# Optimization experiments

Hardware: AMD Instinct MI355X
Metric: run time of the kernel (lower is better)

Reference implementation:

```python
import jax, jax.numpy as jnp
import numpy as np

N_TOKENS = 4096
HIDDEN = 1024
FFN = 2048
N_EXPERTS = 8
TOP_K = 2


def setup_inputs() -> dict:
    key = jax.random.key(0)
    k1, k2, k3, k4 = jax.random.split(key, 4)
    x = jax.random.normal(k1, (N_TOKENS, HIDDEN), dtype=jnp.float32)
    router_weight = jax.random.normal(k2, (HIDDEN, N_EXPERTS), dtype=jnp.float32)
    # matches torch.randn(...) * 0.02 init scale
    w1 = jax.random.normal(k3, (HIDDEN, FFN * N_EXPERTS), dtype=jnp.float32) * 0.02
    w2 = jax.random.normal(k4, (FFN * N_EXPERTS, HIDDEN), dtype=jnp.float32) * 0.02
    return {"x": x, "router_weight": router_weight, "w1": w1, "w2": w2, "top_k": TOP_K}


def reference(x, router_weight, w1, w2, top_k):
    # x: [N, H]; router_weight: [H, E]; w1: [H, E*F]; w2: [E*F, H]
    N, H = x.shape
    E = router_weight.shape[1]
    F = w1.shape[1] // E

    # --- routing (router in fp32, softmax over experts, top-k probs) ---
    logits = x.astype(jnp.float32) @ router_weight            # [N, E]
    probs = jax.nn.softmax(logits, axis=-1)                   # [N, E]
    topk_probs, topk_idx = jax.lax.top_k(probs, top_k)        # [N, k]

    # --- expert FFN: per-expert gelu(x @ w1_e) @ w2_e ---
    # Dense formulation: compute every expert for every token, then gather the
    # top-k outputs per token. Same math as grouped-GEMM dispatch/combine.
    h = jax.nn.gelu(x @ w1, approximate=False)                # [N, E*F]
    h = h.reshape(N, E, F)
    w2e = w2.reshape(E, F, H)
    y = jnp.einsum('nef,efh->neh', h, w2e)                    # [N, E, H]

    # --- combine: weight selected expert outputs by router probs, sum top-k ---
    sel = jnp.take_along_axis(y, topk_idx[:, :, None], axis=1)   # [N, k, H]
    out = (sel * topk_probs[:, :, None].astype(sel.dtype)).sum(axis=1)  # [N, H]
    return out
```

## Files before the change

kernel.cpp:

```cpp
#include <hip/hip_runtime.h>
#include <hip/hip_bf16.h>
#include <math.h>

#define N_TOK 4096
#define HID   1024
#define FFN   2048
#define NEXP  8
#define WROW  (NEXP*FFN)
#define NSLOT (N_TOK*2)
#define NCHUNK (NSLOT/64)

typedef __attribute__((ext_vector_type(4))) float f32x4;
typedef __attribute__((ext_vector_type(8))) short short8;

__device__ inline unsigned short f2bf(float f) {
  union { float f; unsigned u; } v; v.f = f;
  unsigned r = v.u + 0x7fffu + ((v.u >> 16) & 1u);
  return (unsigned short)(r >> 16);
}

__device__ __forceinline__ void gload16(const void* g, void* l) {
  __builtin_amdgcn_global_load_lds((const __attribute__((address_space(1))) void*)g,
                                   (__attribute__((address_space(3))) void*)l, 16, 0, 0);
}

__global__ __launch_bounds__(256) void router_kernel(
    const float* __restrict__ x, const float* __restrict__ rw,
    int* __restrict__ eidx, float* __restrict__ probs,
    unsigned short* __restrict__ xb) {
  __shared__ float rwT[NEXP][HID];
  const int t = threadIdx.x;
  #pragma unroll
  for (int it = 0; it < 8; ++it) {
    const int flat = t * 4 + it * 1024;
    const f32x4 v = *(const f32x4*)&rw[flat];
    #pragma unroll
    for (int j = 0; j < 4; ++j) rwT[(flat + j) & 7][(flat + j) >> 3] = v[j];
  }
  __syncthreads();

  const int w = t >> 6, l = t & 63;
  const int n = blockIdx.x * 4 + w;
  const float* xr = x + (size_t)n * HID;
  float acc[NEXP];
  #pragma unroll
  for (int e = 0; e < NEXP; ++e) acc[e] = 0.f;

  #pragma unroll
  for (int j = 0; j < 4; ++j) {
    const int i = l * 4 + j * 256;
    const f32x4 xv = *(const f32x4*)&xr[i];
    if (xb) {
      ushort4 o;
      o.x = f2bf(xv[0]); o.y = f2bf(xv[1]); o.z = f2bf(xv[2]); o.w = f2bf(xv[3]);
      *(ushort4*)&xb[(size_t)n * HID + i] = o;
    }
    #pragma unroll
    for (int e = 0; e < NEXP; ++e) {
      const f32x4 wv = *(const f32x4*)&rwT[e][i];
      acc[e] += xv[0] * wv[0] + xv[1] * wv[1] + xv[2] * wv[2] + xv[3] * wv[3];
    }
  }
  #pragma unroll
  for (int e = 0; e < NEXP; ++e) {
    float s = acc[e];
    #pragma unroll
    for (int off = 32; off; off >>= 1) s += __shfl_xor(s, off);
    acc[e] = s;
  }
  if (l == 0) {
    float m = acc[0];
    #pragma unroll
    for (int e = 1; e < NEXP; ++e) m = fmaxf(m, acc[e]);
    float p[NEXP]; float den = 0.f;
    #pragma unroll
    for (int e = 0; e < NEXP; ++e) { p[e] = expf(acc[e] - m); den += p[e]; }
    const float inv = 1.f / den;
    int e1 = 0; float b1 = -1.f;
    #pragma unroll
    for (int e = 0; e < NEXP; ++e) if (p[e] > b1) { b1 = p[e]; e1 = e; }
    int e2 = 0; float b2 = -1.f;
    #pragma unroll
    for (int e = 0; e < NEXP; ++e) if (e != e1 && p[e] > b2) { b2 = p[e]; e2 = e; }
    eidx[n * 2 + 0] = e1; eidx[n * 2 + 1] = e2;
    probs[n * 2 + 0] = b1 * inv; probs[n * 2 + 1] = b2 * inv;
  }
}

__global__ __launch_bounds__(256) void dispatch_kernel(
    const int* __restrict__ eidx, const float* __restrict__ probs,
    int* __restrict__ counts, int* __restrict__ offs,
    int* __restrict__ rowtok, float* __restrict__ rowprob) {
  __shared__ int chunkbase[NCHUNK][NEXP];
  __shared__ int tot[NEXP], off_s[NEXP];
  const int t = threadIdx.x;
  const int w = t >> 6, l = t & 63;

  for (int c = w; c < NCHUNK; c += 4) {
    const int e = eidx[c * 64 + l];
    #pragma unroll
    for (int xp = 0; xp < NEXP; ++xp) {
      const unsigned long long m = __ballot(e == xp);
      if (l == xp) chunkbase[c][xp] = __popcll(m);
    }
  }
  __syncthreads();

  if (t < NEXP) {
    int a = 0;
    for (int c = 0; c < NCHUNK; ++c) {
      const int v = chunkbase[c][t];
      chunkbase[c][t] = a;
      a += v;
    }
    tot[t] = a;
  }
  __syncthreads();
  if (t == 0) {
    int a = 0;
    for (int e = 0; e < NEXP; ++e) { off_s[e] = a; offs[e] = a; counts[e] = tot[e]; a += tot[e]; }
  }
  __syncthreads();

  for (int c = w; c < NCHUNK; c += 4) {
    const int s = c * 64 + l;
    const int e = eidx[s];
    unsigned long long mask_e = 0;
    #pragma unroll
    for (int xp = 0; xp < NEXP; ++xp) {
      const unsigned long long m = __ballot(e == xp);
      if (e == xp) mask_e = m;
    }
    const unsigned long long below = mask_e & ((1ull << l) - 1ull);
    const int pos = off_s[e] + chunkbase[c][e] + __popcll(below);
    rowtok[pos]  = s >> 1;
    rowprob[pos] = probs[s];
  }
}

__global__ __launch_bounds__(256) void tconv_kernel(
    const float* __restrict__ in, unsigned short* __restrict__ out,
    int R, int C, int RB) {
  __shared__ float tile[64][65];
  const int r0 = blockIdx.y * 64, c0 = blockIdx.x * 64;
  const int t = threadIdx.x;
  const int tr = t >> 4;
  const int tc4 = (t & 15) * 4;
  #pragma unroll
  for (int i = 0; i < 4; ++i) {
    const int r = tr + i * 16;
    const f32x4 v = *(const f32x4*)&in[(size_t)(r0 + r) * C + c0 + tc4];
    tile[r][tc4 + 0] = v[0]; tile[r][tc4 + 1] = v[1];
    tile[r][tc4 + 2] = v[2]; tile[r][tc4 + 3] = v[3];
  }
  __syncthreads();
  const int eb  = r0 / RB;
  const int rm0 = r0 % RB;
  #pragma unroll
  for (int i = 0; i < 4; ++i) {
    const int c = tr + i * 16;
    ushort4 o;
    o.x = f2bf(tile[tc4 + 0][c]); o.y = f2bf(tile[tc4 + 1][c]);
    o.z = f2bf(tile[tc4 + 2][c]); o.w = f2bf(tile[tc4 + 3][c]);
    const size_t oidx = (size_t)eb * C * RB + (size_t)(c0 + c) * RB + rm0 + tc4;
    *(ushort4*)&out[oidx] = o;
  }
}

__global__ __launch_bounds__(256) void gemm1_fast(
    const unsigned short* __restrict__ xb, const unsigned short* __restrict__ w1t,
    const int* __restrict__ rowtok, const int* __restrict__ counts,
    const int* __restrict__ offs, unsigned short* __restrict__ h1) {
  const int e   = blockIdx.z;
  const int cnt = counts[e];
  const int m0  = blockIdx.y * 128;
  if (m0 >= cnt) return;
  const int n0  = blockIdx.x * 128;
  const int seg = offs[e];

  __shared__ alignas(16) unsigned short Al[128 * 32];
  __shared__ alignas(16) unsigned short Bl[128 * 32];

  const int t  = threadIdx.x;
  const int l  = t & 63;
  const int w  = t >> 6;
  const int wr = w >> 1, wc = w & 1;
  const int lr = l & 15, hi = l >> 4;

  const int rowS = t >> 2;
  const int kc   = (t & 3) * 8;
  const int ra0 = m0 + rowS      < cnt ? m0 + rowS      : cnt - 1;
  const int ra1 = m0 + rowS + 64 < cnt ? m0 + rowS + 64 : cnt - 1;
  const unsigned short* aptr0 = xb + (size_t)rowtok[seg + ra0] * HID + kc;
  const unsigned short* aptr1 = xb + (size_t)rowtok[seg + ra1] * HID + kc;
  const unsigned short* bptr0 = w1t + ((size_t)e * FFN + n0 + rowS)      * HID + kc;
  const unsigned short* bptr1 = w1t + ((size_t)e * FFN + n0 + rowS + 64) * HID + kc;
  unsigned short* const ldsA0 = Al + (t & 192) * 8;
  unsigned short* const ldsB0 = Bl + (t & 192) * 8;

  f32x4 acc[4][4];
  #pragma unroll
  for (int i = 0; i < 4; ++i)
    #pragma unroll
    for (int j = 0; j < 4; ++j) acc[i][j] = (f32x4){0.f, 0.f, 0.f, 0.f};

  for (int k0 = 0; k0 < HID; k0 += 32) {
    gload16(aptr0 + k0, ldsA0);
    gload16(aptr1 + k0, ldsA0 + 2048);
    gload16(bptr0 + k0, ldsB0);
    gload16(bptr1 + k0, ldsB0 + 2048);
    __syncthreads();
    short8 af[4], bfr[4];
    #pragma unroll
    for (int mi = 0; mi < 4; ++mi) af[mi]  = *(const short8*)&Al[(wr * 64 + mi * 16 + lr) * 32 + hi * 8];
    #pragma unroll
    for (int ni = 0; ni < 4; ++ni) bfr[ni] = *(const short8*)&Bl[(wc * 64 + ni * 16 + lr) * 32 + hi * 8];
    #pragma unroll
    for (int mi = 0; mi < 4; ++mi)
      #pragma unroll
      for (int ni = 0; ni < 4; ++ni)
        acc[mi][ni] = __builtin_amdgcn_mfma_f32_16x16x32_bf16(af[mi], bfr[ni], acc[mi][ni], 0, 0, 0);
    __syncthreads();
  }

  #pragma unroll
  for (int mi = 0; mi < 4; ++mi) {
    #pragma unroll
    for (int r = 0; r < 4; ++r) {
      const int grow = m0 + wr * 64 + mi * 16 + hi * 4 + r;
      if (grow < cnt) {
        const size_t rowoff = (size_t)(seg + grow) * FFN + n0 + wc * 64 + lr;
        #pragma unroll
        for (int ni = 0; ni < 4; ++ni) {
          const float v = acc[mi][ni][r];
          const float g = 0.5f * v * (1.0f + erff(v * 0.70710678118654752f));
          h1[rowoff + ni * 16] = f2bf(g);
        }
      }
    }
  }
}

__global__ __launch_bounds__(256) void gemm2_fast(
    const unsigned short* __restrict__ h1, const unsigned short* __restrict__ w2t,
    const int* __restrict__ rowtok, const float* __restrict__ rowprob,
    const int* __restrict__ counts, const int* __restrict__ offs,
    float* __restrict__ out) {
  const int e   = blockIdx.z;
  const int cnt = counts[e];
  const int m0  = blockIdx.y * 128;
  if (m0 >= cnt) return;
  const int n0  = blockIdx.x * 128;
  const int seg = offs[e];

  __shared__ alignas(16) unsigned short Al[128 * 32];
  __shared__ alignas(16) unsigned short Bl[128 * 32];

  const int t  = threadIdx.x;
  const int l  = t & 63;
  const int w  = t >> 6;
  const int wr = w >> 1, wc = w & 1;
  const int lr = l & 15, hi = l >> 4;

  const int rowS = t >> 2;
  const int kc   = (t & 3) * 8;
  const int ra0 = m0 + rowS      < cnt ? m0 + rowS      : cnt - 1;
  const int ra1 = m0 + rowS + 64 < cnt ? m0 + rowS + 64 : cnt - 1;
  const unsigned short* aptr0 = h1 + (size_t)(seg + ra0) * FFN + kc;
  const unsigned short* aptr1 = h1 + (size_t)(seg + ra1) * FFN + kc;
  const unsigned short* bptr0 = w2t + ((size_t)e * HID + n0 + rowS)      * FFN + kc;
  const unsigned short* bptr1 = w2t + ((size_t)e * HID + n0 + rowS + 64) * FFN + kc;
  unsigned short* const ldsA0 = Al + (t & 192) * 8;
  unsigned short* const ldsB0 = Bl + (t & 192) * 8;

  f32x4 acc[4][4];
  #pragma unroll
  for (int i = 0; i < 4; ++i)
    #pragma unroll
    for (int j = 0; j < 4; ++j) acc[i][j] = (f32x4){0.f, 0.f, 0.f, 0.f};

  for (int k0 = 0; k0 < FFN; k0 += 32) {
    gload16(aptr0 + k0, ldsA0);
    gload16(aptr1 + k0, ldsA0 + 2048);
    gload16(bptr0 + k0, ldsB0);
    gload16(bptr1 + k0, ldsB0 + 2048);
    __syncthreads();
    short8 af[4], bfr[4];
    #pragma unroll
    for (int mi = 0; mi < 4; ++mi) af[mi]  = *(const short8*)&Al[(wr * 64 + mi * 16 + lr) * 32 + hi * 8];
    #pragma unroll
    for (int ni = 0; ni < 4; ++ni) bfr[ni] = *(const short8*)&Bl[(wc * 64 + ni * 16 + lr) * 32 + hi * 8];
    #pragma unroll
    for (int mi = 0; mi < 4; ++mi)
      #pragma unroll
      for (int ni = 0; ni < 4; ++ni)
        acc[mi][ni] = __builtin_amdgcn_mfma_f32_16x16x32_bf16(af[mi], bfr[ni], acc[mi][ni], 0, 0, 0);
    __syncthreads();
  }

  #pragma unroll
  for (int mi = 0; mi < 4; ++mi) {
    #pragma unroll
    for (int r = 0; r < 4; ++r) {
      const int grow = m0 + wr * 64 + mi * 16 + hi * 4 + r;
      if (grow < cnt) {
        const int slot = seg + grow;
        const int tok  = rowtok[slot];
        const float p  = rowprob[slot];
        #pragma unroll
        for (int ni = 0; ni < 4; ++ni)
          atomicAdd(&out[(size_t)tok * HID + n0 + wc * 64 + ni * 16 + lr], p * acc[mi][ni][r]);
      }
    }
  }
}

__global__ __launch_bounds__(256) void gemm1_old(
    const float* __restrict__ x, const float* __restrict__ w1,
    const int* __restrict__ rowtok, const int* __restrict__ counts,
    const int* __restrict__ offs, unsigned short* __restrict__ h1) {
  const int e   = blockIdx.z;
  const int cnt = counts[e];
  const int m0  = blockIdx.y * 64;
  if (m0 >= cnt) return;
  const int n0  = blockIdx.x * 64;
  const int seg = offs[e];
  __shared__ unsigned short Al[64 * 40];
  __shared__ unsigned short Bl[64 * 40];
  const int t  = threadIdx.x;
  const int l  = t & 63;
  const int wv = t >> 6;
  const int wr = wv >> 1, wc = wv & 1;
  const int am  = t >> 2;
  const int akb = (t & 3) * 8;
  const int amg = m0 + am;
  const bool aval = (amg < cnt);
  const float* aptr = aval ? (x + (size_t)rowtok[seg + amg] * HID + akb) : x;
  const int bn  = t & 63;
  const int bkg = (t >> 6) * 8;
  const float* bptr = w1 + (size_t)e * FFN + n0 + bn;
  f32x4 acc[2][2];
  #pragma unroll
  for (int i = 0; i < 2; ++i)
    #pragma unroll
    for (int j = 0; j < 2; ++j) acc[i][j] = (f32x4){0.f, 0.f, 0.f, 0.f};
  const int kreg = (l >> 4) * 8;
  const int lr   = l & 15;
  for (int k0 = 0; k0 < HID; k0 += 32) {
    short8 av = (short8){0,0,0,0,0,0,0,0};
    if (aval) {
      const f32x4 v0 = *(const f32x4*)(aptr + k0);
      const f32x4 v1 = *(const f32x4*)(aptr + k0 + 4);
      #pragma unroll
      for (int j = 0; j < 4; ++j) { av[j] = (short)f2bf(v0[j]); av[4 + j] = (short)f2bf(v1[j]); }
    }
    *(short8*)&Al[am * 40 + akb] = av;
    short8 bv;
    #pragma unroll
    for (int j = 0; j < 8; ++j) bv[j] = (short)f2bf(bptr[(size_t)(k0 + bkg + j) * WROW]);
    *(short8*)&Bl[bn * 40 + bkg] = bv;
    __syncthreads();
    short8 af[2], bfr[2];
    #pragma unroll
    for (int mi = 0; mi < 2; ++mi) af[mi]  = *(const short8*)&Al[(wr * 32 + mi * 16 + lr) * 40 + kreg];
    #pragma unroll
    for (int ni = 0; ni < 2; ++ni) bfr[ni] = *(const short8*)&Bl[(wc * 32 + ni * 16 + lr) * 40 + kreg];
    #pragma unroll
    for (int mi = 0; mi < 2; ++mi)
      #pragma unroll
      for (int ni = 0; ni < 2; ++ni)
        acc[mi][ni] = __builtin_amdgcn_mfma_f32_16x16x32_bf16(af[mi], bfr[ni], acc[mi][ni], 0, 0, 0);
    __syncthreads();
  }
  const int kq = l >> 4;
  #pragma unroll
  for (int mi = 0; mi < 2; ++mi) {
    #pragma unroll
    for (int r = 0; r < 4; ++r) {
      const int grow = m0 + wr * 32 + mi * 16 + kq * 4 + r;
      if (grow < cnt) {
        #pragma unroll
        for (int ni = 0; ni < 2; ++ni) {
          const float v = acc[mi][ni][r];
          const float g = 0.5f * v * (1.0f + erff(v * 0.70710678118654752f));
          h1[(size_t)(seg + grow) * FFN + n0 + wc * 32 + ni * 16 + lr] = f2bf(g);
        }
      }
    }
  }
}

__global__ __launch_bounds__(256) void gemm2_old(
    const unsigned short* __restrict__ h1, const float* __restrict__ w2,
    const int* __restrict__ rowtok, const float* __restrict__ rowprob,
    const int* __restrict__ counts, const int* __restrict__ offs,
    float* __restrict__ out) {
  const int e   = blockIdx.z;
  const int cnt = counts[e];
  const int m0  = blockIdx.y * 64;
  if (m0 >= cnt) return;
  const int n0  = blockIdx.x * 64;
  const int seg = offs[e];
  __shared__ unsigned short Al[64 * 40];
  __shared__ unsigned short Bl[64 * 40];
  const int t  = threadIdx.x;
  const int l  = t & 63;
  const int wv = t >> 6;
  const int wr = wv >> 1, wc = wv & 1;
  const int am  = t >> 2;
  const int akb = (t & 3) * 8;
  const int amg = m0 + am;
  const bool aval = (amg < cnt);
  const unsigned short* aptr = aval ? (h1 + (size_t)(seg + amg) * FFN + akb) : h1;
  const int bn  = t & 63;
  const int bkg = (t >> 6) * 8;
  const float* bptr = w2 + (size_t)e * FFN * HID + n0 + bn;
  f32x4 acc[2][2];
  #pragma unroll
  for (int i = 0; i < 2; ++i)
    #pragma unroll
    for (int j = 0; j < 2; ++j) acc[i][j] = (f32x4){0.f, 0.f, 0.f, 0.f};
  const int kreg = (l >> 4) * 8;
  const int lr   = l & 15;
  for (int k0 = 0; k0 < FFN; k0 += 32) {
    short8 av = (short8){0,0,0,0,0,0,0,0};
    if (aval) av = *(const short8*)(aptr + k0);
    *(short8*)&Al[am * 40 + akb] = av;
    short8 bv;
    #pragma unroll
    for (int j = 0; j < 8; ++j) bv[j] = (short)f2bf(bptr[(size_t)(k0 + bkg + j) * HID]);
    *(short8*)&Bl[bn * 40 + bkg] = bv;
    __syncthreads();
    short8 af[2], bfr[2];
    #pragma unroll
    for (int mi = 0; mi < 2; ++mi) af[mi]  = *(const short8*)&Al[(wr * 32 + mi * 16 + lr) * 40 + kreg];
    #pragma unroll
    for (int ni = 0; ni < 2; ++ni) bfr[ni] = *(const short8*)&Bl[(wc * 32 + ni * 16 + lr) * 40 + kreg];
    #pragma unroll
    for (int mi = 0; mi < 2; ++mi)
      #pragma unroll
      for (int ni = 0; ni < 2; ++ni)
        acc[mi][ni] = __builtin_amdgcn_mfma_f32_16x16x32_bf16(af[mi], bfr[ni], acc[mi][ni], 0, 0, 0);
    __syncthreads();
  }
  const int kq = l >> 4;
  #pragma unroll
  for (int mi = 0; mi < 2; ++mi) {
    #pragma unroll
    for (int r = 0; r < 4; ++r) {
      const int grow = m0 + wr * 32 + mi * 16 + kq * 4 + r;
      if (grow < cnt) {
        const int slot = seg + grow;
        const int tok  = rowtok[slot];
        const float p  = rowprob[slot];
        #pragma unroll
        for (int ni = 0; ni < 2; ++ni)
          atomicAdd(&out[(size_t)tok * HID + n0 + wc * 32 + ni * 16 + lr], p * acc[mi][ni][r]);
      }
    }
  }
}

extern "C" void kernel_launch(void* const* d_in, const int* in_sizes, int n_in,
                              void* d_out, int out_size, void* d_ws, size_t ws_size,
                              hipStream_t stream) {
  const float* x  = (const float*)d_in[0];
  const float* rw = (const float*)d_in[1];
  const float* w1 = (const float*)d_in[2];
  const float* w2 = (const float*)d_in[3];
  float* out = (float*)d_out;

  int*   counts  = (int*)d_ws;
  int*   cursors = counts + 8;
  int*   offs    = counts + 16;
  int*   eidx    = counts + 32;
  float* probs   = (float*)(eidx + NSLOT);
  int*   rowtok  = (int*)(probs + NSLOT);
  float* rowprob = (float*)(rowtok + NSLOT);
  unsigned short* h1 = (unsigned short*)(rowprob + NSLOT);
  unsigned short* xb = h1 + (size_t)NSLOT * FFN;
  unsigned short* wt = xb + (size_t)N_TOK * HID;
  const size_t need_fast = (size_t)((char*)(wt + (size_t)WROW * HID) - (char*)d_ws);
  const bool fast = (ws_size >= need_fast);
  (void)cursors;

  hipMemsetAsync(d_out, 0, (size_t)out_size * sizeof(float), stream);

  router_kernel<<<N_TOK / 4, 256, 0, stream>>>(x, rw, eidx, probs, fast ? xb : nullptr);
  dispatch_kernel<<<1, 256, 0, stream>>>(eidx, probs, counts, offs, rowtok, rowprob);

  if (fast) {
    tconv_kernel<<<dim3(WROW / 64, HID / 64), 256, 0, stream>>>(w1, wt, HID, WROW, HID);
    gemm1_fast<<<dim3(FFN / 128, NSLOT / 128, NEXP), 256, 0, stream>>>(xb, wt, rowtok, counts, offs, h1);
    tconv_kernel<<<dim3(HID / 64, WROW / 64), 256, 0, stream>>>(w2, wt, WROW, HID, FFN);
    gemm2_fast<<<dim3(HID / 128, NSLOT / 128, NEXP), 256, 0, stream>>>(h1, wt, rowtok, rowprob, counts, offs, out);
  } else {
    gemm1_old<<<dim3(FFN / 64, NSLOT / 64, NEXP), 256, 0, stream>>>(x, w1, rowtok, counts, offs, h1);
    gemm2_old<<<dim3(HID / 64, NSLOT / 64, NEXP), 256, 0, stream>>>(h1, w2, rowtok, rowprob, counts, offs, out);
  }
}
```

Measured before the change: 223.5 us.

## Double-buffer LDS in both expert GEMMs and split-K gemm2 across two halves

Both grouped GEMM kernels now use two LDS buffers, so the global-to-LDS loads for the next K slice are issued while MFMAs run on the current slice. This hides memory latency that the single-buffer loop exposed behind a barrier. gemm2 also splits its K dimension (FFN) into two halves across the grid z dimension, doubling block count to improve occupancy. The existing atomicAdd epilogue combines the partial sums, at the cost of twice the atomic traffic on the output.

```diff
diff --git a/kernel.cpp b/kernel.cpp
--- a/kernel.cpp
+++ b/kernel.cpp
@@ -178,8 +178,8 @@
   const int n0  = blockIdx.x * 128;
   const int seg = offs[e];
 
-  __shared__ alignas(16) unsigned short Al[128 * 32];
-  __shared__ alignas(16) unsigned short Bl[128 * 32];
+  __shared__ alignas(16) unsigned short Al[2][128 * 32];
+  __shared__ alignas(16) unsigned short Bl[2][128 * 32];
 
   const int t  = threadIdx.x;
   const int l  = t & 63;
@@ -195,8 +195,7 @@
   const unsigned short* aptr1 = xb + (size_t)rowtok[seg + ra1] * HID + kc;
   const unsigned short* bptr0 = w1t + ((size_t)e * FFN + n0 + rowS)      * HID + kc;
   const unsigned short* bptr1 = w1t + ((size_t)e * FFN + n0 + rowS + 64) * HID + kc;
-  unsigned short* const ldsA0 = Al + (t & 192) * 8;
-  unsigned short* const ldsB0 = Bl + (t & 192) * 8;
+  const int ldst = (t & 192) * 8;
 
   f32x4 acc[4][4];
   #pragma unroll
@@ -204,22 +203,33 @@
     #pragma unroll
     for (int j = 0; j < 4; ++j) acc[i][j] = (f32x4){0.f, 0.f, 0.f, 0.f};
 
-  for (int k0 = 0; k0 < HID; k0 += 32) {
-    gload16(aptr0 + k0, ldsA0);
-    gload16(aptr1 + k0, ldsA0 + 2048);
-    gload16(bptr0 + k0, ldsB0);
-    gload16(bptr1 + k0, ldsB0 + 2048);
-    __syncthreads();
+  auto STAGE = [&](int b, int k0) {
+    gload16(aptr0 + k0, &Al[b][ldst]);
+    gload16(aptr1 + k0, &Al[b][ldst + 2048]);
+    gload16(bptr0 + k0, &Bl[b][ldst]);
+    gload16(bptr1 + k0, &Bl[b][ldst + 2048]);
+  };
+  auto COMPUTE = [&](int b) {
     short8 af[4], bfr[4];
     #pragma unroll
-    for (int mi = 0; mi < 4; ++mi) af[mi]  = *(const short8*)&Al[(wr * 64 + mi * 16 + lr) * 32 + hi * 8];
-    #pragma unroll
-    for (int ni = 0; ni < 4; ++ni) bfr[ni] = *(const short8*)&Bl[(wc * 64 + ni * 16 + lr) * 32 + hi * 8];
+    for (int mi = 0; mi < 4; ++mi) af[mi]  = *(const short8*)&Al[b][(wr * 64 + mi * 16 + lr) * 32 + hi * 8];
+    #pragma unroll
+    for (int ni = 0; ni < 4; ++ni) bfr[ni] = *(const short8*)&Bl[b][(wc * 64 + ni * 16 + lr) * 32 + hi * 8];
     #pragma unroll
     for (int mi = 0; mi < 4; ++mi)
       #pragma unroll
       for (int ni = 0; ni < 4; ++ni)
         acc[mi][ni] = __builtin_amdgcn_mfma_f32_16x16x32_bf16(af[mi], bfr[ni], acc[mi][ni], 0, 0, 0);
+  };
+
+  STAGE(0, 0);
+  __syncthreads();
+  for (int k0 = 0; k0 < HID; k0 += 64) {
+    STAGE(1, k0 + 32);
+    COMPUTE(0);
+    __syncthreads();
+    if (k0 + 64 < HID) STAGE(0, k0 + 64);
+    COMPUTE(1);
     __syncthreads();
   }
 
@@ -246,15 +256,17 @@
     const int* __restrict__ rowtok, const float* __restrict__ rowprob,
     const int* __restrict__ counts, const int* __restrict__ offs,
     float* __restrict__ out) {
-  const int e   = blockIdx.z;
+  const int e   = blockIdx.z & 7;
+  const int kz  = blockIdx.z >> 3;
   const int cnt = counts[e];
   const int m0  = blockIdx.y * 128;
   if (m0 >= cnt) return;
   const int n0  = blockIdx.x * 128;
   const int seg = offs[e];
-
-  __shared__ alignas(16) unsigned short Al[128 * 32];
-  __shared__ alignas(16) unsigned short Bl[128 * 32];
+  const int kbase = kz * (FFN / 2);
+
+  __shared__ alignas(16) unsigned short Al[2][128 * 32];
+  __shared__ alignas(16) unsigned short Bl[2][128 * 32];
 
   const int t  = threadIdx.x;
   const int l  = t & 63;
@@ -266,12 +278,11 @@
   const int kc   = (t & 3) * 8;
   const int ra0 = m0 + rowS      < cnt ? m0 + rowS      : cnt - 1;
   const int ra1 = m0 + rowS + 64 < cnt ? m0 + rowS + 64 : cnt - 1;
-  const unsigned short* aptr0 = h1 + (size_t)(seg + ra0) * FFN + kc;
-  const unsigned short* aptr1 = h1 + (size_t)(seg + ra1) * FFN + kc;
-  const unsigned short* bptr0 = w2t + ((size_t)e * HID + n0 + rowS)      * FFN + kc;
-  const unsigned short* bptr1 = w2t + ((size_t)e * HID + n0 + rowS + 64) * FFN + kc;
-  unsigned short* const ldsA0 = Al + (t & 192) * 8;
-  unsigned short* const ldsB0 = Bl + (t & 192) * 8;
+  const unsigned short* aptr0 = h1 + (size_t)(seg + ra0) * FFN + kbase + kc;
+  const unsigned short* aptr1 = h1 + (size_t)(seg + ra1) * FFN + kbase + kc;
+  const unsigned short* bptr0 = w2t + ((size_t)e * HID + n0 + rowS)      * FFN + kbase + kc;
+  const unsigned short* bptr1 = w2t + ((size_t)e * HID + n0 + rowS + 64) * FFN + kbase + kc;
+  const int ldst = (t & 192) * 8;
 
   f32x4 acc[4][4];
   #pragma unroll
@@ -279,22 +290,34 @@
     #pragma unroll
     for (int j = 0; j < 4; ++j) acc[i][j] = (f32x4){0.f, 0.f, 0.f, 0.f};
 
-  for (int k0 = 0; k0 < FFN; k0 += 32) {
-    gload16(aptr0 + k0, ldsA0);
-    gload16(aptr1 + k0, ldsA0 + 2048);
-    gload16(bptr0 + k0, ldsB0);
-    gload16(bptr1 + k0, ldsB0 + 2048);
-    __syncthreads();
+  auto STAGE = [&](int b, int k0) {
+    gload16(aptr0 + k0, &Al[b][ldst]);
+    gload16(aptr1 + k0, &Al[b][ldst + 2048]);
+    gload16(bptr0 + k0, &Bl[b][ldst]);
+    gload16(bptr1 + k0, &Bl[b][ldst + 2048]);
+  };
+  auto COMPUTE = [&](int b) {
     short8 af[4], bfr[4];
     #pragma unroll
-    for (int mi = 0; mi < 4; ++mi) af[mi]  = *(const short8*)&Al[(wr * 64 + mi * 16 + lr) * 32 + hi * 8];
-    #pragma unroll
-    for (int ni = 0; ni < 4; ++ni) bfr[ni] = *(const short8*)&Bl[(wc * 64 + ni * 16 + lr) * 32 + hi * 8];
+    for (int mi = 0; mi < 4; ++mi) af[mi]  = *(const short8*)&Al[b][(wr * 64 + mi * 16 + lr) * 32 + hi * 8];
+    #pragma unroll
+    for (int ni = 0; ni < 4; ++ni) bfr[ni] = *(const short8*)&Bl[b][(wc * 64 + ni * 16 + lr) * 32 + hi * 8];
     #pragma unroll
     for (int mi = 0; mi < 4; ++mi)
       #pragma unroll
       for (int ni = 0; ni < 4; ++ni)
         acc[mi][ni] = __builtin_amdgcn_mfma_f32_16x16x32_bf16(af[mi], bfr[ni], acc[mi][ni], 0, 0, 0);
+  };
+
+  STAGE(0, 0);
+  __syncthreads();
+  const int KLEN = FFN / 2;
+  for (int k0 = 0; k0 < KLEN; k0 += 64) {
+    STAGE(1, k0 + 32);
+    COMPUTE(0);
+    __syncthreads();
+    if (k0 + 64 < KLEN) STAGE(0, k0 + 64);
+    COMPUTE(1);
     __syncthreads();
   }
 
@@ -493,7 +516,7 @@
     tconv_kernel<<<dim3(WROW / 64, HID / 64), 256, 0, stream>>>(w1, wt, HID, WROW, HID);
     gemm1_fast<<<dim3(FFN / 128, NSLOT / 128, NEXP), 256, 0, stream>>>(xb, wt, rowtok, counts, offs, h1);
     tconv_kernel<<<dim3(HID / 64, WROW / 64), 256, 0, stream>>>(w2, wt, WROW, HID, FFN);
-    gemm2_fast<<<dim3(HID / 128, NSLOT / 128, NEXP), 256, 0, stream>>>(h1, wt, rowtok, rowprob, counts, offs, out);
+    gemm2_fast<<<dim3(HID / 128, NSLOT / 128, NEXP * 2), 256, 0, stream>>>(h1, wt, rowtok, rowprob, counts, offs, out);
   } else {
     gemm1_old<<<dim3(FFN / 64, NSLOT / 64, NEXP), 256, 0, stream>>>(x, w1, rowtok, counts, offs, h1);
     gemm2_old<<<dim3(HID / 64, NSLOT / 64, NEXP), 256, 0, stream>>>(h1, w2, rowtok, rowprob, counts, offs, out);
```

Measured after the change: 252.9 us. 1.13x slower.

## Replace atomic scatter in expert GEMM2 with split-K bf16 partials and combine kernel

Applied to the files above, without the earlier changes.

The second expert GEMM now writes per-slot bf16 partial outputs, with K split in two for more blocks, instead of atomically adding into the output. A new combine kernel gathers each token's two slots through a token-to-slot map, weights them by the router probabilities and writes the output directly, so the output memset is no longer needed. This removes fp32 atomic contention and raises the block count for the GEMM. It costs an extra launch and extra workspace traffic, and rounding partials to bf16 adds error.

```diff
diff --git a/kernel.cpp b/kernel.cpp
--- a/kernel.cpp
+++ b/kernel.cpp
@@ -18,6 +18,9 @@
   unsigned r = v.u + 0x7fffu + ((v.u >> 16) & 1u);
   return (unsigned short)(r >> 16);
 }
+__device__ __forceinline__ float bf2f(unsigned short u) {
+  union { unsigned u; float f; } v; v.u = ((unsigned)u) << 16; return v.f;
+}
 
 __device__ __forceinline__ void gload16(const void* g, void* l) {
   __builtin_amdgcn_global_load_lds((const __attribute__((address_space(1))) void*)g,
@@ -90,7 +93,8 @@
 __global__ __launch_bounds__(256) void dispatch_kernel(
     const int* __restrict__ eidx, const float* __restrict__ probs,
     int* __restrict__ counts, int* __restrict__ offs,
-    int* __restrict__ rowtok, float* __restrict__ rowprob) {
+    int* __restrict__ rowtok, float* __restrict__ rowprob,
+    int* __restrict__ tokslot) {
   __shared__ int chunkbase[NCHUNK][NEXP];
   __shared__ int tot[NEXP], off_s[NEXP];
   const int t = threadIdx.x;
@@ -135,6 +139,7 @@
     const int pos = off_s[e] + chunkbase[c][e] + __popcll(below);
     rowtok[pos]  = s >> 1;
     rowprob[pos] = probs[s];
+    tokslot[s]   = pos;
   }
 }
 
@@ -241,7 +246,104 @@
   }
 }
 
+template<int KS>
 __global__ __launch_bounds__(256) void gemm2_fast(
+    const unsigned short* __restrict__ h1, const unsigned short* __restrict__ w2t,
+    const int* __restrict__ counts, const int* __restrict__ offs,
+    unsigned short* __restrict__ y) {
+  const int e   = blockIdx.z & 7;
+  const int kz  = blockIdx.z >> 3;
+  const int cnt = counts[e];
+  const int m0  = blockIdx.y * 128;
+  if (m0 >= cnt) return;
+  const int n0  = blockIdx.x * 128;
+  const int seg = offs[e];
+  constexpr int KLEN = FFN / KS;
+  const int kbase = kz * KLEN;
+
+  __shared__ alignas(16) unsigned short Al[128 * 32];
+  __shared__ alignas(16) unsigned short Bl[128 * 32];
+
+  const int t  = threadIdx.x;
+  const int l  = t & 63;
+  const int w  = t >> 6;
+  const int wr = w >> 1, wc = w & 1;
+  const int lr = l & 15, hi = l >> 4;
+
+  const int rowS = t >> 2;
+  const int kc   = (t & 3) * 8;
+  const int ra0 = m0 + rowS      < cnt ? m0 + rowS      : cnt - 1;
+  const int ra1 = m0 + rowS + 64 < cnt ? m0 + rowS + 64 : cnt - 1;
+  const unsigned short* aptr0 = h1 + (size_t)(seg + ra0) * FFN + kbase + kc;
+  const unsigned short* aptr1 = h1 + (size_t)(seg + ra1) * FFN + kbase + kc;
+  const unsigned short* bptr0 = w2t + ((size_t)e * HID + n0 + rowS)      * FFN + kbase + kc;
+  const unsigned short* bptr1 = w2t + ((size_t)e * HID + n0 + rowS + 64) * FFN + kbase + kc;
+  unsigned short* const ldsA0 = Al + (t & 192) * 8;
+  unsigned short* const ldsB0 = Bl + (t & 192) * 8;
+
+  f32x4 acc[4][4];
+  #pragma unroll
+  for (int i = 0; i < 4; ++i)
+    #pragma unroll
+    for (int j = 0; j < 4; ++j) acc[i][j] = (f32x4){0.f, 0.f, 0.f, 0.f};
+
+  for (int k0 = 0; k0 < KLEN; k0 += 32) {
+    gload16(aptr0 + k0, ldsA0);
+    gload16(aptr1 + k0, ldsA0 + 2048);
+    gload16(bptr0 + k0, ldsB0);
+    gload16(bptr1 + k0, ldsB0 + 2048);
+    __syncthreads();
+    short8 af[4], bfr[4];
+    #pragma unroll
+    for (int mi = 0; mi < 4; ++mi) af[mi]  = *(const short8*)&Al[(wr * 64 + mi * 16 + lr) * 32 + hi * 8];
+    #pragma unroll
+    for (int ni = 0; ni < 4; ++ni) bfr[ni] = *(const short8*)&Bl[(wc * 64 + ni * 16 + lr) * 32 + hi * 8];
+    #pragma unroll
+    for (int mi = 0; mi < 4; ++mi)
+      #pragma unroll
+      for (int ni = 0; ni < 4; ++ni)
+        acc[mi][ni] = __builtin_amdgcn_mfma_f32_16x16x32_bf16(af[mi], bfr[ni], acc[mi][ni], 0, 0, 0);
+    __syncthreads();
+  }
+
+  #pragma unroll
+  for (int mi = 0; mi < 4; ++mi) {
+    #pragma unroll
+    for (int r = 0; r < 4; ++r) {
+      const int grow = m0 + wr * 64 + mi * 16 + hi * 4 + r;
+      if (grow < cnt) {
+        const int slot = seg + grow;
+        unsigned short* yrow = y + ((size_t)kz * NSLOT + slot) * HID + n0 + wc * 64 + lr;
+        #pragma unroll
+        for (int ni = 0; ni < 4; ++ni)
+          yrow[ni * 16] = f2bf(acc[mi][ni][r]);
+      }
+    }
+  }
+}
+
+template<int KS>
+__global__ __launch_bounds__(256) void combine_kernel(
+    const unsigned short* __restrict__ y, const int* __restrict__ tokslot,
+    const float* __restrict__ probs, float* __restrict__ out) {
+  const int n = blockIdx.x;
+  const int c = threadIdx.x * 4;
+  const int s1 = tokslot[n * 2 + 0], s2 = tokslot[n * 2 + 1];
+  const float p1 = probs[n * 2 + 0], p2 = probs[n * 2 + 1];
+  float r0 = 0.f, r1 = 0.f, r2 = 0.f, r3 = 0.f;
+  #pragma unroll
+  for (int kz = 0; kz < KS; ++kz) {
+    const ushort4 a = *(const ushort4*)&y[((size_t)kz * NSLOT + s1) * HID + c];
+    const ushort4 b = *(const ushort4*)&y[((size_t)kz * NSLOT + s2) * HID + c];
+    r0 += p1 * bf2f(a.x) + p2 * bf2f(b.x);
+    r1 += p1 * bf2f(a.y) + p2 * bf2f(b.y);
+    r2 += p1 * bf2f(a.z) + p2 * bf2f(b.z);
+    r3 += p1 * bf2f(a.w) + p2 * bf2f(b.w);
+  }
+  *(f32x4*)&out[(size_t)n * HID + c] = (f32x4){r0, r1, r2, r3};
+}
+
+__global__ __launch_bounds__(256) void gemm2_fast_atomic(
     const unsigned short* __restrict__ h1, const unsigned short* __restrict__ w2t,
     const int* __restrict__ rowtok, const float* __restrict__ rowprob,
     const int* __restrict__ counts, const int* __restrict__ offs,
@@ -471,30 +573,41 @@
   float* out = (float*)d_out;
 
   int*   counts  = (int*)d_ws;
-  int*   cursors = counts + 8;
-  int*   offs    = counts + 16;
-  int*   eidx    = counts + 32;
+  int*   offs    = counts + 8;
+  int*   tokslot = counts + 16;
+  int*   eidx    = tokslot + NSLOT;
   float* probs   = (float*)(eidx + NSLOT);
   int*   rowtok  = (int*)(probs + NSLOT);
   float* rowprob = (float*)(rowtok + NSLOT);
   unsigned short* h1 = (unsigned short*)(rowprob + NSLOT);
   unsigned short* xb = h1 + (size_t)NSLOT * FFN;
   unsigned short* wt = xb + (size_t)N_TOK * HID;
-  const size_t need_fast = (size_t)((char*)(wt + (size_t)WROW * HID) - (char*)d_ws);
-  const bool fast = (ws_size >= need_fast);
-  (void)cursors;
-
-  hipMemsetAsync(d_out, 0, (size_t)out_size * sizeof(float), stream);
+  unsigned short* y  = wt + (size_t)WROW * HID;
+
+  const size_t need_base = (size_t)((char*)y - (char*)d_ws);
+  const size_t need_y1   = need_base + (size_t)NSLOT * HID * 2;
+  const size_t need_y2   = need_base + (size_t)2 * NSLOT * HID * 2;
+  const bool fast = (ws_size >= need_base);
 
   router_kernel<<<N_TOK / 4, 256, 0, stream>>>(x, rw, eidx, probs, fast ? xb : nullptr);
-  dispatch_kernel<<<1, 256, 0, stream>>>(eidx, probs, counts, offs, rowtok, rowprob);
+  dispatch_kernel<<<1, 256, 0, stream>>>(eidx, probs, counts, offs, rowtok, rowprob, tokslot);
 
   if (fast) {
     tconv_kernel<<<dim3(WROW / 64, HID / 64), 256, 0, stream>>>(w1, wt, HID, WROW, HID);
     gemm1_fast<<<dim3(FFN / 128, NSLOT / 128, NEXP), 256, 0, stream>>>(xb, wt, rowtok, counts, offs, h1);
     tconv_kernel<<<dim3(HID / 64, WROW / 64), 256, 0, stream>>>(w2, wt, WROW, HID, FFN);
-    gemm2_fast<<<dim3(HID / 128, NSLOT / 128, NEXP), 256, 0, stream>>>(h1, wt, rowtok, rowprob, counts, offs, out);
+    if (ws_size >= need_y2) {
+      gemm2_fast<2><<<dim3(HID / 128, NSLOT / 128, NEXP * 2), 256, 0, stream>>>(h1, wt, counts, offs, y);
+      combine_kernel<2><<<N_TOK, 256, 0, stream>>>(y, tokslot, probs, out);
+    } else if (ws_size >= need_y1) {
+      gemm2_fast<1><<<dim3(HID / 128, NSLOT / 128, NEXP), 256, 0, stream>>>(h1, wt, counts, offs, y);
+      combine_kernel<1><<<N_TOK, 256, 0, stream>>>(y, tokslot, probs, out);
+    } else {
+      hipMemsetAsync(d_out, 0, (size_t)out_size * sizeof(float), stream);
+      gemm2_fast_atomic<<<dim3(HID / 128, NSLOT / 128, NEXP), 256, 0, stream>>>(h1, wt, rowtok, rowprob, counts, offs, out);
+    }
   } else {
+    hipMemsetAsync(d_out, 0, (size_t)out_size * sizeof(float), stream);
     gemm1_old<<<dim3(FFN / 64, NSLOT / 64, NEXP), 256, 0, stream>>>(x, w1, rowtok, counts, offs, h1);
     gemm2_old<<<dim3(HID / 64, NSLOT / 64, NEXP), 256, 0, stream>>>(h1, w2, rowtok, rowprob, counts, offs, out);
   }
```

Result: no change. 223.1 us (-0.2%).
